# Kernel tuning notes

Measured on AMD Instinct MI355X. Metric: run time of the kernel, lower is better.

The kernel has to match this reference:

```python
import jax, jax.numpy as jnp
import numpy as np

B, T, D = 4, 4096, 512
K = 8192  # codebook_size


def setup_inputs() -> dict:
    key = jax.random.key(0)
    k1, k2 = jax.random.split(key)
    x = jax.random.normal(k1, (B, T, D), dtype=jnp.float32)
    embed = jax.random.normal(k2, (K, D), dtype=jnp.float32)
    return {"x": x, "embed": embed}


def reference(x, embed):
    # preprocess: flatten all leading dims -> [N, D]
    shape = x.shape
    xf = x.reshape(-1, shape[-1])  # [N, D]
    # quantize: negative squared euclidean distance, argmax over codebook
    x_sq = jnp.sum(xf * xf, axis=1, keepdims=True)          # [N, 1]
    e_sq = jnp.sum(embed * embed, axis=1)[None, :]          # [1, K]
    dist = -(x_sq - 2.0 * (xf @ embed.T) + e_sq)            # [N, K]
    embed_ind = jnp.argmax(dist, axis=-1)                   # [N]
    embed_ind = embed_ind.reshape(shape[:-1])               # [B, T]
    quantize = embed[embed_ind]                             # [B, T, D]
    return (quantize, embed_ind)
```

## Files before the change

### kernel.cpp

```cpp
#include <hip/hip_runtime.h>
#include <cstddef>
#include <cstdint>

typedef unsigned short ushort_t;
typedef unsigned long long ull_t;
typedef __attribute__((ext_vector_type(8))) short short8;
typedef __attribute__((ext_vector_type(4))) float f32x4;

constexpr int D_ = 512, K_ = 8192, N_ = 16384;
constexpr float MARGIN = 0.75f;

__device__ __forceinline__ ushort_t f2bf(float f) {
  unsigned u = __float_as_uint(f);
  return (ushort_t)((u + 0x7FFFu + ((u >> 16) & 1u)) >> 16);
}
__device__ __forceinline__ unsigned flipf(float s) {
  unsigned u = __float_as_uint(s);
  return (u & 0x80000000u) ? ~u : (u | 0x80000000u);
}
__device__ __forceinline__ float unflipf(unsigned m) {
  unsigned u = (m & 0x80000000u) ? (m ^ 0x80000000u) : ~m;
  return __uint_as_float(u);
}
__device__ __forceinline__ ull_t umax64(ull_t a, ull_t b) { return a > b ? a : b; }
__device__ __forceinline__ ull_t umin64(ull_t a, ull_t b) { return a < b ? a : b; }

__global__ __launch_bounds__(256) void conv_all(const float* __restrict__ x,
                                                const float* __restrict__ e,
                                                char* __restrict__ xbt, char* __restrict__ ebt,
                                                float* __restrict__ ehs) {
  const int g = threadIdx.x & 15, rr = threadIdx.x >> 4;
  if ((int)blockIdx.x < 1024) {
    const int tile = blockIdx.x >> 3, rg = blockIdx.x & 7;
    const int r = rg * 16 + rr;
    const float4* src = (const float4*)(x + ((size_t)(tile * 128 + r)) * D_ + g * 32);
    float4 f[8];
#pragma unroll
    for (int q = 0; q < 8; ++q) f[q] = src[q];
    char* dbase = xbt + (size_t)tile * 131072 + g * 8192 + r * 16;
#pragma unroll
    for (int kq = 0; kq < 4; ++kq) {
      float4 a = f[kq * 2], b = f[kq * 2 + 1];
      short8 v;
      v[0] = (short)f2bf(a.x); v[1] = (short)f2bf(a.y); v[2] = (short)f2bf(a.z); v[3] = (short)f2bf(a.w);
      v[4] = (short)f2bf(b.x); v[5] = (short)f2bf(b.y); v[6] = (short)f2bf(b.z); v[7] = (short)f2bf(b.w);
      *(short8*)(dbase + kq * 2048) = v;
    }
  } else {
    const int bid = blockIdx.x - 1024;
    const int tile = bid >> 3, rg = bid & 7;
    const int r = rg * 16 + rr;
    const int col = tile * 128 + r;
    const float4* src = (const float4*)(e + (size_t)col * D_ + g * 32);
    float4 f[8];
    float ss = 0.f;
#pragma unroll
    for (int q = 0; q < 8; ++q) {
      f[q] = src[q];
      ss += f[q].x * f[q].x + f[q].y * f[q].y + f[q].z * f[q].z + f[q].w * f[q].w;
    }
    char* dbase = ebt + (size_t)tile * 131072 + g * 8192 + r * 16;
#pragma unroll
    for (int kq = 0; kq < 4; ++kq) {
      float4 a = f[kq * 2], b = f[kq * 2 + 1];
      short8 v;
      v[0] = (short)f2bf(a.x); v[1] = (short)f2bf(a.y); v[2] = (short)f2bf(a.z); v[3] = (short)f2bf(a.w);
      v[4] = (short)f2bf(b.x); v[5] = (short)f2bf(b.y); v[6] = (short)f2bf(b.z); v[7] = (short)f2bf(b.w);
      *(short8*)(dbase + kq * 2048) = v;
    }
#pragma unroll
    for (int m = 1; m < 16; m <<= 1) ss += __shfl_xor(ss, m);
    if (g == 0) ehs[col] = 0.5f * ss;
  }
}

__global__ __launch_bounds__(256, 4) void dist_mfma(const char* __restrict__ xbt,
                                                    const char* __restrict__ ebt,
                                                    const float* __restrict__ ehs,
                                                    ull_t* __restrict__ ppu,
                                                    float* __restrict__ pps2) {
  __shared__ ull_t lp[256];
  __shared__ float ls2[256];
  const int tid = threadIdx.x, w = tid >> 6, l = tid & 63;
  const int fid = blockIdx.x + blockIdx.y * 128;
  const int k8 = fid & 7, j = fid >> 3;
  const int by = k8 * 8 + (j & 7), bx = j >> 3;
  const int row0 = bx * 128, col0 = by * 128;
  const int wr = w >> 1, wc = w & 1;
  const char* abase = xbt + (size_t)bx * 131072 + (l >> 4) * 2048 + wr * 1024 + (l & 15) * 16;
  const char* bbase = ebt + (size_t)by * 131072 + (l >> 4) * 2048 + wc * 1024 + (l & 15) * 16;

  f32x4 acc[4][4] = {};
#pragma unroll 4
  for (int g = 0; g < 16; ++g) {
    short8 a[4], b[4];
#pragma unroll
    for (int i = 0; i < 4; ++i)
      a[i] = *(const short8*)(abase + g * 8192 + i * 256);
#pragma unroll
    for (int jj = 0; jj < 4; ++jj)
      b[jj] = *(const short8*)(bbase + g * 8192 + jj * 256);
#pragma unroll
    for (int i = 0; i < 4; ++i)
#pragma unroll
      for (int jj = 0; jj < 4; ++jj)
        acc[i][jj] = __builtin_amdgcn_mfma_f32_16x16x32_bf16(a[i], b[jj], acc[i][jj], 0, 0, 0);
  }

  float eh[4];
  unsigned ic[4];
#pragma unroll
  for (int jj = 0; jj < 4; ++jj) {
    int col = col0 + wc * 64 + jj * 16 + (l & 15);
    eh[jj] = ehs[col];
    ic[jj] = 0xFFFFFFFFu - (unsigned)col;
  }
#pragma unroll
  for (int i = 0; i < 4; ++i)
#pragma unroll
    for (int jj = 0; jj < 4; ++jj)
#pragma unroll
      for (int r = 0; r < 4; ++r)
        acc[i][jj][r] -= eh[jj];

  float mx[4][4];
#pragma unroll
  for (int i = 0; i < 4; ++i)
#pragma unroll
    for (int r = 0; r < 4; ++r)
      mx[i][r] = fmaxf(fmaxf(acc[i][0][r], acc[i][1][r]), fmaxf(acc[i][2][r], acc[i][3][r]));
#pragma unroll
  for (int m = 1; m < 16; m <<= 1)
#pragma unroll
    for (int i = 0; i < 4; ++i)
#pragma unroll
      for (int r = 0; r < 4; ++r)
        mx[i][r] = fmaxf(mx[i][r], __shfl_xor(mx[i][r], m));

  unsigned ii[4][4];
#pragma unroll
  for (int i = 0; i < 4; ++i)
#pragma unroll
    for (int r = 0; r < 4; ++r) {
      unsigned t0 = (acc[i][0][r] == mx[i][r]) ? ic[0] : 0u;
      unsigned t1 = (acc[i][1][r] == mx[i][r]) ? ic[1] : 0u;
      unsigned t2 = (acc[i][2][r] == mx[i][r]) ? ic[2] : 0u;
      unsigned t3 = (acc[i][3][r] == mx[i][r]) ? ic[3] : 0u;
      unsigned u01 = t0 > t1 ? t0 : t1, u23 = t2 > t3 ? t2 : t3;
      ii[i][r] = u01 > u23 ? u01 : u23;
    }
#pragma unroll
  for (int m = 1; m < 16; m <<= 1)
#pragma unroll
    for (int i = 0; i < 4; ++i)
#pragma unroll
      for (int r = 0; r < 4; ++r) {
        unsigned o = __shfl_xor(ii[i][r], m);
        ii[i][r] = ii[i][r] > o ? ii[i][r] : o;
      }

  float s2[4][4];
#pragma unroll
  for (int i = 0; i < 4; ++i)
#pragma unroll
    for (int r = 0; r < 4; ++r) {
      float t0 = (ic[0] == ii[i][r]) ? -3e38f : acc[i][0][r];
      float t1 = (ic[1] == ii[i][r]) ? -3e38f : acc[i][1][r];
      float t2 = (ic[2] == ii[i][r]) ? -3e38f : acc[i][2][r];
      float t3 = (ic[3] == ii[i][r]) ? -3e38f : acc[i][3][r];
      s2[i][r] = fmaxf(fmaxf(t0, t1), fmaxf(t2, t3));
    }
#pragma unroll
  for (int m = 1; m < 16; m <<= 1)
#pragma unroll
    for (int i = 0; i < 4; ++i)
#pragma unroll
      for (int r = 0; r < 4; ++r)
        s2[i][r] = fmaxf(s2[i][r], __shfl_xor(s2[i][r], m));

  const int c = l & 15, g16 = l >> 4;
  float fs1 = -3e38f, fs2 = -3e38f;
  unsigned fii = 0;
#pragma unroll
  for (int i = 0; i < 4; ++i) {
    if ((c >> 2) == i) {
      int rsel = c & 3;
      fs1 = (rsel == 0) ? mx[i][0] : (rsel == 1) ? mx[i][1] : (rsel == 2) ? mx[i][2] : mx[i][3];
      fii = (rsel == 0) ? ii[i][0] : (rsel == 1) ? ii[i][1] : (rsel == 2) ? ii[i][2] : ii[i][3];
      fs2 = (rsel == 0) ? s2[i][0] : (rsel == 1) ? s2[i][1] : (rsel == 2) ? s2[i][2] : s2[i][3];
    }
  }
  ull_t fp = ((ull_t)flipf(fs1) << 32) | fii;
  const int rib = wr * 64 + (c >> 2) * 16 + g16 * 4 + (c & 3);

  lp[wc * 128 + rib] = fp; ls2[wc * 128 + rib] = fs2;
  __syncthreads();
  if (wc == 0) {
    ull_t op = lp[128 + rib];
    float os2 = ls2[128 + rib];
    ull_t lo = umin64(fp, op);
    fs2 = fmaxf(fmaxf(fs2, os2), unflipf((unsigned)(lo >> 32)));
    fp = umax64(fp, op);
    ppu[(size_t)(row0 + rib) * 64 + by] = fp;
    pps2[(size_t)(row0 + rib) * 64 + by] = fs2;
  }
}

__global__ __launch_bounds__(256) void finalize(const float* __restrict__ x,
                                                const float* __restrict__ embed,
                                                const float* __restrict__ ehs,
                                                const ull_t* __restrict__ ppu,
                                                const float* __restrict__ pps2,
                                                float* __restrict__ out) {
  const int row = (blockIdx.x * 256 + threadIdx.x) >> 6;
  const int l = threadIdx.x & 63;
  ull_t p = ppu[(size_t)row * 64 + l];
  float s2 = pps2[(size_t)row * 64 + l];
  ull_t gp = p;
#pragma unroll
  for (int m = 1; m < 64; m <<= 1) gp = umax64(gp, __shfl_xor(gp, m));
  float gs = unflipf((unsigned)(gp >> 32));
  float t = gs - MARGIN;
  bool cand = (unflipf((unsigned)(p >> 32)) >= t);
  bool ovf = (s2 >= t);
  ull_t b1 = __ballot(cand);
  ull_t b2 = __ballot(ovf);
  int idx;
  if (__popcll(b1) == 1 && b2 == 0ull) {
    idx = (int)(0xFFFFFFFFu - (unsigned)(gp & 0xFFFFFFFFu));
  } else {
    const float4* xr4 = (const float4*)(x + (size_t)row * D_ + l * 8);
    float4 xa = xr4[0], xc = xr4[1];
    ull_t best = 0ull;
    ull_t bb = b1;
    while (bb) {
      int b = (int)__builtin_ctzll(bb);
      bb &= bb - 1;
      ull_t pb = __shfl(p, b);
      int col = (int)(0xFFFFFFFFu - (unsigned)(pb & 0xFFFFFFFFu));
      const float4* er4 = (const float4*)(embed + (size_t)col * D_ + l * 8);
      float4 ea = er4[0], ec = er4[1];
      float s = xa.x * ea.x + xa.y * ea.y + xa.z * ea.z + xa.w * ea.w
              + xc.x * ec.x + xc.y * ec.y + xc.z * ec.z + xc.w * ec.w;
#pragma unroll
      for (int m = 1; m < 64; m <<= 1) s += __shfl_xor(s, m);
      s -= ehs[col];
      best = umax64(best, ((ull_t)flipf(s) << 32) | (0xFFFFFFFFu - (unsigned)col));
    }
    while (b2) {
      int b = (int)__builtin_ctzll(b2);
      b2 &= b2 - 1;
      int c0 = b * 128;
      const float* xr = x + (size_t)row * D_;
      const float* e0p = embed + (size_t)(c0 + l) * D_;
      const float* e1p = embed + (size_t)(c0 + 64 + l) * D_;
      float a0 = 0.f, a1 = 0.f;
      for (int d = 0; d < D_; d += 4) {
        float4 xv = *(const float4*)(xr + d);
        float4 v0 = *(const float4*)(e0p + d);
        float4 v1 = *(const float4*)(e1p + d);
        a0 = fmaf(v0.x, xv.x, fmaf(v0.y, xv.y, fmaf(v0.z, xv.z, fmaf(v0.w, xv.w, a0))));
        a1 = fmaf(v1.x, xv.x, fmaf(v1.y, xv.y, fmaf(v1.z, xv.z, fmaf(v1.w, xv.w, a1))));
      }
      float s0 = a0 - ehs[c0 + l];
      float s1 = a1 - ehs[c0 + 64 + l];
      ull_t p0 = ((ull_t)flipf(s0) << 32) | (0xFFFFFFFFu - (unsigned)(c0 + l));
      ull_t p1 = ((ull_t)flipf(s1) << 32) | (0xFFFFFFFFu - (unsigned)(c0 + 64 + l));
      ull_t pk = umax64(p0, p1);
#pragma unroll
      for (int m = 1; m < 64; m <<= 1) pk = umax64(pk, __shfl_xor(pk, m));
      best = umax64(best, pk);
    }
    idx = (int)(0xFFFFFFFFu - (unsigned)(best & 0xFFFFFFFFu));
  }
  const float4* src = (const float4*)(embed + (size_t)idx * D_);
  float4* dst = (float4*)(out + (size_t)row * D_);
  dst[l] = src[l];
  dst[l + 64] = src[l + 64];
  if (l == 0) out[(size_t)N_ * D_ + row] = (float)idx;
}

extern "C" void kernel_launch(void* const* d_in, const int* in_sizes, int n_in,
                              void* d_out, int out_size, void* d_ws, size_t ws_size,
                              hipStream_t stream) {
  const float* x = (const float*)d_in[0];
  const float* e = (const float*)d_in[1];
  float* out = (float*)d_out;

  char* ws = (char*)d_ws;
  char* xbt = ws;
  char* ebt = ws + 16777216;
  float* ehs = (float*)(ws + 25165824);
  ull_t* ppu = (ull_t*)(ws + 25198592);
  float* pps2 = (float*)(ws + 33587200);

  conv_all<<<1536, 256, 0, stream>>>(x, e, xbt, ebt, ehs);
  dist_mfma<<<dim3(128, 64), 256, 0, stream>>>(xbt, ebt, ehs, ppu, pps2);
  finalize<<<4096, 256, 0, stream>>>(x, e, ehs, ppu, pps2, out);
}
```

Measured before the change: 215.0 us.

## Widen distance tile to 128x256 per block with MFMA priority hints

Each dist_mfma block now covers 256 codebook columns instead of 128, with every wave computing a 64x128 sub-tile (4x8 MFMA accumulators). A-fragment loads are reused across twice as many columns, and the grid and the per-row partial count are halved. The partial buffers, the finalize reduction (now 32 lanes) and the exact-recompute fallback are updated to match. The larger accumulator set pushes occupancy down to 2 blocks per CU, and s_setprio is placed around the MFMA loop to favour the matrix issue.

```diff
diff --git a/kernel.cpp b/kernel.cpp
--- a/kernel.cpp
+++ b/kernel.cpp
@@ -74,7 +74,7 @@
   }
 }
 
-__global__ __launch_bounds__(256, 4) void dist_mfma(const char* __restrict__ xbt,
+__global__ __launch_bounds__(256, 2) void dist_mfma(const char* __restrict__ xbt,
                                                     const char* __restrict__ ebt,
                                                     const float* __restrict__ ehs,
                                                     ull_t* __restrict__ ppu,
@@ -84,41 +84,43 @@
   const int tid = threadIdx.x, w = tid >> 6, l = tid & 63;
   const int fid = blockIdx.x + blockIdx.y * 128;
   const int k8 = fid & 7, j = fid >> 3;
-  const int by = k8 * 8 + (j & 7), bx = j >> 3;
-  const int row0 = bx * 128, col0 = by * 128;
+  const int by = k8 * 4 + (j & 3), bx = j >> 2;
+  const int row0 = bx * 128, col0 = by * 256;
   const int wr = w >> 1, wc = w & 1;
   const char* abase = xbt + (size_t)bx * 131072 + (l >> 4) * 2048 + wr * 1024 + (l & 15) * 16;
-  const char* bbase = ebt + (size_t)by * 131072 + (l >> 4) * 2048 + wc * 1024 + (l & 15) * 16;
-
-  f32x4 acc[4][4] = {};
-#pragma unroll 4
+  const char* bbase = ebt + (size_t)(by * 2 + wc) * 131072 + (l >> 4) * 2048 + (l & 15) * 16;
+
+  f32x4 acc[4][8] = {};
+#pragma unroll
   for (int g = 0; g < 16; ++g) {
-    short8 a[4], b[4];
+    short8 a[4], b[8];
 #pragma unroll
     for (int i = 0; i < 4; ++i)
       a[i] = *(const short8*)(abase + g * 8192 + i * 256);
 #pragma unroll
-    for (int jj = 0; jj < 4; ++jj)
+    for (int jj = 0; jj < 8; ++jj)
       b[jj] = *(const short8*)(bbase + g * 8192 + jj * 256);
-#pragma unroll
-    for (int i = 0; i < 4; ++i)
-#pragma unroll
-      for (int jj = 0; jj < 4; ++jj)
+    __builtin_amdgcn_s_setprio(1);
+#pragma unroll
+    for (int i = 0; i < 4; ++i)
+#pragma unroll
+      for (int jj = 0; jj < 8; ++jj)
         acc[i][jj] = __builtin_amdgcn_mfma_f32_16x16x32_bf16(a[i], b[jj], acc[i][jj], 0, 0, 0);
-  }
-
-  float eh[4];
-  unsigned ic[4];
-#pragma unroll
-  for (int jj = 0; jj < 4; ++jj) {
-    int col = col0 + wc * 64 + jj * 16 + (l & 15);
+    __builtin_amdgcn_s_setprio(0);
+  }
+
+  float eh[8];
+  unsigned ic[8];
+#pragma unroll
+  for (int jj = 0; jj < 8; ++jj) {
+    int col = col0 + wc * 128 + jj * 16 + (l & 15);
     eh[jj] = ehs[col];
     ic[jj] = 0xFFFFFFFFu - (unsigned)col;
   }
 #pragma unroll
   for (int i = 0; i < 4; ++i)
 #pragma unroll
-    for (int jj = 0; jj < 4; ++jj)
+    for (int jj = 0; jj < 8; ++jj)
 #pragma unroll
       for (int r = 0; r < 4; ++r)
         acc[i][jj][r] -= eh[jj];
@@ -127,8 +129,13 @@
 #pragma unroll
   for (int i = 0; i < 4; ++i)
 #pragma unroll
-    for (int r = 0; r < 4; ++r)
-      mx[i][r] = fmaxf(fmaxf(acc[i][0][r], acc[i][1][r]), fmaxf(acc[i][2][r], acc[i][3][r]));
+    for (int r = 0; r < 4; ++r) {
+      float m01 = fmaxf(acc[i][0][r], acc[i][1][r]);
+      float m23 = fmaxf(acc[i][2][r], acc[i][3][r]);
+      float m45 = fmaxf(acc[i][4][r], acc[i][5][r]);
+      float m67 = fmaxf(acc[i][6][r], acc[i][7][r]);
+      mx[i][r] = fmaxf(fmaxf(m01, m23), fmaxf(m45, m67));
+    }
 #pragma unroll
   for (int m = 1; m < 16; m <<= 1)
 #pragma unroll
@@ -142,12 +149,13 @@
   for (int i = 0; i < 4; ++i)
 #pragma unroll
     for (int r = 0; r < 4; ++r) {
-      unsigned t0 = (acc[i][0][r] == mx[i][r]) ? ic[0] : 0u;
-      unsigned t1 = (acc[i][1][r] == mx[i][r]) ? ic[1] : 0u;
-      unsigned t2 = (acc[i][2][r] == mx[i][r]) ? ic[2] : 0u;
-      unsigned t3 = (acc[i][3][r] == mx[i][r]) ? ic[3] : 0u;
-      unsigned u01 = t0 > t1 ? t0 : t1, u23 = t2 > t3 ? t2 : t3;
-      ii[i][r] = u01 > u23 ? u01 : u23;
+      unsigned u = 0u;
+#pragma unroll
+      for (int jj = 0; jj < 8; ++jj) {
+        unsigned t = (acc[i][jj][r] == mx[i][r]) ? ic[jj] : 0u;
+        u = u > t ? u : t;
+      }
+      ii[i][r] = u;
     }
 #pragma unroll
   for (int m = 1; m < 16; m <<= 1)
@@ -164,11 +172,13 @@
   for (int i = 0; i < 4; ++i)
 #pragma unroll
     for (int r = 0; r < 4; ++r) {
-      float t0 = (ic[0] == ii[i][r]) ? -3e38f : acc[i][0][r];
-      float t1 = (ic[1] == ii[i][r]) ? -3e38f : acc[i][1][r];
-      float t2 = (ic[2] == ii[i][r]) ? -3e38f : acc[i][2][r];
-      float t3 = (ic[3] == ii[i][r]) ? -3e38f : acc[i][3][r];
-      s2[i][r] = fmaxf(fmaxf(t0, t1), fmaxf(t2, t3));
+      float v = -3e38f;
+#pragma unroll
+      for (int jj = 0; jj < 8; ++jj) {
+        float t = (ic[jj] == ii[i][r]) ? -3e38f : acc[i][jj][r];
+        v = fmaxf(v, t);
+      }
+      s2[i][r] = v;
     }
 #pragma unroll
   for (int m = 1; m < 16; m <<= 1)
@@ -201,8 +211,8 @@
     ull_t lo = umin64(fp, op);
     fs2 = fmaxf(fmaxf(fs2, os2), unflipf((unsigned)(lo >> 32)));
     fp = umax64(fp, op);
-    ppu[(size_t)(row0 + rib) * 64 + by] = fp;
-    pps2[(size_t)(row0 + rib) * 64 + by] = fs2;
+    ppu[(size_t)(row0 + rib) * 32 + by] = fp;
+    pps2[(size_t)(row0 + rib) * 32 + by] = fs2;
   }
 }
 
@@ -214,15 +224,17 @@
                                                 float* __restrict__ out) {
   const int row = (blockIdx.x * 256 + threadIdx.x) >> 6;
   const int l = threadIdx.x & 63;
-  ull_t p = ppu[(size_t)row * 64 + l];
-  float s2 = pps2[(size_t)row * 64 + l];
+  ull_t p = 0;
+  float s2 = -3e38f;
+  if (l < 32) { p = ppu[(size_t)row * 32 + l]; s2 = pps2[(size_t)row * 32 + l]; }
   ull_t gp = p;
 #pragma unroll
   for (int m = 1; m < 64; m <<= 1) gp = umax64(gp, __shfl_xor(gp, m));
   float gs = unflipf((unsigned)(gp >> 32));
   float t = gs - MARGIN;
-  bool cand = (unflipf((unsigned)(p >> 32)) >= t);
-  bool ovf = (s2 >= t);
+  float s1 = unflipf((unsigned)(p >> 32));
+  bool cand = (l < 32) && (s1 >= t);
+  bool ovf = (l < 32) && (s2 >= t);
   ull_t b1 = __ballot(cand);
   ull_t b2 = __ballot(ovf);
   int idx;
@@ -250,23 +262,28 @@
     while (b2) {
       int b = (int)__builtin_ctzll(b2);
       b2 &= b2 - 1;
-      int c0 = b * 128;
+      int c0 = b * 256;
       const float* xr = x + (size_t)row * D_;
       const float* e0p = embed + (size_t)(c0 + l) * D_;
       const float* e1p = embed + (size_t)(c0 + 64 + l) * D_;
-      float a0 = 0.f, a1 = 0.f;
+      const float* e2p = embed + (size_t)(c0 + 128 + l) * D_;
+      const float* e3p = embed + (size_t)(c0 + 192 + l) * D_;
+      float a0 = 0.f, a1 = 0.f, a2 = 0.f, a3 = 0.f;
       for (int d = 0; d < D_; d += 4) {
         float4 xv = *(const float4*)(xr + d);
         float4 v0 = *(const float4*)(e0p + d);
         float4 v1 = *(const float4*)(e1p + d);
+        float4 v2 = *(const float4*)(e2p + d);
+        float4 v3 = *(const float4*)(e3p + d);
         a0 = fmaf(v0.x, xv.x, fmaf(v0.y, xv.y, fmaf(v0.z, xv.z, fmaf(v0.w, xv.w, a0))));
         a1 = fmaf(v1.x, xv.x, fmaf(v1.y, xv.y, fmaf(v1.z, xv.z, fmaf(v1.w, xv.w, a1))));
+        a2 = fmaf(v2.x, xv.x, fmaf(v2.y, xv.y, fmaf(v2.z, xv.z, fmaf(v2.w, xv.w, a2))));
+        a3 = fmaf(v3.x, xv.x, fmaf(v3.y, xv.y, fmaf(v3.z, xv.z, fmaf(v3.w, xv.w, a3))));
       }
-      float s0 = a0 - ehs[c0 + l];
-      float s1 = a1 - ehs[c0 + 64 + l];
-      ull_t p0 = ((ull_t)flipf(s0) << 32) | (0xFFFFFFFFu - (unsigned)(c0 + l));
-      ull_t p1 = ((ull_t)flipf(s1) << 32) | (0xFFFFFFFFu - (unsigned)(c0 + 64 + l));
-      ull_t pk = umax64(p0, p1);
+      ull_t pk = ((ull_t)flipf(a0 - ehs[c0 + l]) << 32) | (0xFFFFFFFFu - (unsigned)(c0 + l));
+      pk = umax64(pk, ((ull_t)flipf(a1 - ehs[c0 + 64 + l]) << 32) | (0xFFFFFFFFu - (unsigned)(c0 + 64 + l)));
+      pk = umax64(pk, ((ull_t)flipf(a2 - ehs[c0 + 128 + l]) << 32) | (0xFFFFFFFFu - (unsigned)(c0 + 128 + l)));
+      pk = umax64(pk, ((ull_t)flipf(a3 - ehs[c0 + 192 + l]) << 32) | (0xFFFFFFFFu - (unsigned)(c0 + 192 + l)));
 #pragma unroll
       for (int m = 1; m < 64; m <<= 1) pk = umax64(pk, __shfl_xor(pk, m));
       best = umax64(best, pk);
@@ -292,9 +309,9 @@
   char* ebt = ws + 16777216;
   float* ehs = (float*)(ws + 25165824);
   ull_t* ppu = (ull_t*)(ws + 25198592);
-  float* pps2 = (float*)(ws + 33587200);
+  float* pps2 = (float*)(ws + 29392896);
 
   conv_all<<<1536, 256, 0, stream>>>(x, e, xbt, ebt, ehs);
-  dist_mfma<<<dim3(128, 64), 256, 0, stream>>>(xbt, ebt, ehs, ppu, pps2);
+  dist_mfma<<<dim3(128, 32), 256, 0, stream>>>(xbt, ebt, ehs, ppu, pps2);
   finalize<<<4096, 256, 0, stream>>>(x, e, ehs, ppu, pps2, out);
 }
```

Result: slower. 226.6 us (+5.4%).
